# Kernel tuning notes

Hardware: AMD Instinct MI355X
Metric: run time of the kernel (lower is better)

Reference implementation:

```python
import jax, jax.numpy as jnp
import numpy as np

B, S, I, H = 64, 512, 256, 512


def setup_inputs() -> dict:
    key = jax.random.key(0)
    k1, k2, k3, k4 = jax.random.split(key, 4)
    scale = 0.1  # torch init uniform(-0.1, 0.1); we use scaled normal for randn fill
    x = jax.random.normal(k1, (B, S, I), dtype=jnp.float32)
    W = jax.random.normal(k2, (I, 4 * H), dtype=jnp.float32) * scale
    U = jax.random.normal(k3, (H, 4 * H), dtype=jnp.float32) * scale
    bias = jax.random.normal(k4, (4 * H,), dtype=jnp.float32) * scale
    return {"x": x, "W": W, "U": U, "bias": bias}


def reference(x, W, U, bias):
    bs, seq_len, _ = x.shape
    hidden = U.shape[0]
    h0 = jnp.zeros((bs, hidden), dtype=x.dtype)
    c0 = jnp.zeros((bs, hidden), dtype=x.dtype)

    # Precompute the input projection for all timesteps in one big GEMM: [B,S,4H]
    x_proj = jnp.einsum("bsi,ig->bsg", x, W) + bias

    def step(carry, xp_t):
        h_t, c_t = carry
        gates = xp_t + h_t @ U  # [B, 4H]
        i_t, f_t, g_t, o_t = jnp.split(gates, 4, axis=1)
        i_t = jax.nn.sigmoid(i_t)
        f_t = jax.nn.sigmoid(f_t)
        g_t = jnp.tanh(g_t)
        o_t = jax.nn.sigmoid(o_t)
        c_t = f_t * c_t + i_t * g_t
        h_t = o_t * jnp.tanh(c_t)
        return (h_t, c_t), h_t

    (h_f, c_f), h_seq = jax.lax.scan(step, (h0, c0), jnp.swapaxes(x_proj, 0, 1))
    hidden_seq = jnp.swapaxes(h_seq, 0, 1)  # [B, S, H]
    # dropout p=0.0 (eval) -> identity
    return hidden_seq, h_f, c_f
```

## Files before the change

### kernel.cpp

```cpp
#include <hip/hip_runtime.h>
#include <hip/hip_bf16.h>


#define BB 64
#define SS 512
#define II 256
#define HH 512
#define G4 2048
#define NGRP 4
#define GB 16
#define NWPG 16
#define NCOL 128
#define NU 32

typedef __attribute__((ext_vector_type(8))) short bf16x8;
typedef __attribute__((ext_vector_type(4))) float f32x4;
typedef unsigned long long u64t;

__device__ __forceinline__ u64t ld_llc_u64(const u64t* p) {
  return __hip_atomic_load((u64t*)p, __ATOMIC_RELAXED,
                           __HIP_MEMORY_SCOPE_AGENT);
}
__device__ __forceinline__ void st_llc_u64(u64t* p, u64t v) {
  __hip_atomic_store(p, v, __ATOMIC_RELAXED, __HIP_MEMORY_SCOPE_AGENT);
}

__global__ void convert_x_kernel(const float* __restrict__ x,
                                 __hip_bfloat16* __restrict__ xb) {
  int blk = blockIdx.x;
  int b = blk >> 9;
  int t = blk & (SS - 1);
  int i = threadIdx.x;
  xb[((size_t)t * BB + b) * II + i] = __float2bfloat16(x[(size_t)blk * II + i]);
}

__global__ void transpose_w_kernel(const float* __restrict__ W,
                                   __hip_bfloat16* __restrict__ Wt) {
  __shared__ __hip_bfloat16 tile[64][64 + 8];
  int kb = blockIdx.x & 3;
  int nb = blockIdx.x >> 2;
  int k0 = kb * 64, nb0 = nb * 64;
#pragma unroll
  for (int p = 0; p < 16; ++p) {
    int r = p * 4 + (threadIdx.x >> 6);
    int c = threadIdx.x & 63;
    tile[r][c] = __float2bfloat16(W[(size_t)(k0 + r) * G4 + nb0 + c]);
  }
  __syncthreads();
#pragma unroll
  for (int p = 0; p < 16; ++p) {
    int n = p * 4 + (threadIdx.x >> 6);
    int k = threadIdx.x & 63;
    Wt[(size_t)(nb0 + n) * II + k0 + k] = tile[k][n];
  }
}

__global__ __launch_bounds__(256, 1)
void lstm_step(const float* __restrict__ U,
               const float* __restrict__ bias,
               const __hip_bfloat16* __restrict__ xb,
               const __hip_bfloat16* __restrict__ Wt,
               u64t* __restrict__ hpub,
               unsigned* cnt,
               float* out) {
  __shared__ alignas(16) __hip_bfloat16 Ut[NCOL][HH + 8];
  __shared__ alignas(16) __hip_bfloat16 hL[GB][HH + 8];
  __shared__ float gate[GB][NCOL + 4];
  __shared__ float bia[NCOL];
  __shared__ int sh_grp, sh_w16, sh_fast;

  const int tid = threadIdx.x;

  if (tid == 0) {
    unsigned xcc;
    asm volatile("s_getreg_b32 %0, hwreg(HW_REG_XCC_ID)" : "=s"(xcc));
    xcc &= 7u;
    unsigned my = __hip_atomic_fetch_add(&cnt[xcc], 1u, __ATOMIC_RELAXED,
                                         __HIP_MEMORY_SCOPE_AGENT);
    __hip_atomic_fetch_add(&cnt[15], 1u, __ATOMIC_RELEASE,
                           __HIP_MEMORY_SCOPE_AGENT);
    while (__hip_atomic_load(&cnt[15], __ATOMIC_ACQUIRE,
                             __HIP_MEMORY_SCOPE_AGENT) < 256u) {}
    unsigned c0 = __hip_atomic_load(&cnt[0], __ATOMIC_RELAXED,
                                    __HIP_MEMORY_SCOPE_AGENT);
    unsigned c1 = __hip_atomic_load(&cnt[1], __ATOMIC_RELAXED,
                                    __HIP_MEMORY_SCOPE_AGENT);
    unsigned c2 = __hip_atomic_load(&cnt[2], __ATOMIC_RELAXED,
                                    __HIP_MEMORY_SCOPE_AGENT);
    unsigned c3 = __hip_atomic_load(&cnt[3], __ATOMIC_RELAXED,
                                    __HIP_MEMORY_SCOPE_AGENT);
    int fast = (c0 >= NWPG && c1 >= NWPG && c2 >= NWPG && c3 >= NWPG);
    int grp = -1, w16 = 0;
    if (fast) {
      if (xcc < NGRP && my < NWPG) { grp = (int)xcc; w16 = (int)my; }
    } else {
      unsigned sp = __hip_atomic_fetch_add(&cnt[9], 1u, __ATOMIC_RELAXED,
                                           __HIP_MEMORY_SCOPE_AGENT);
      if (sp < NGRP * NWPG) { grp = (int)(sp >> 4); w16 = (int)(sp & 15); }
    }
    sh_grp = grp; sh_w16 = w16; sh_fast = fast;
  }
  __syncthreads();
  const int grp = sh_grp;
  const int w16 = sh_w16;
  const bool fast = (bool)sh_fast;
  if (grp < 0) return;
  const int n0 = w16 * NU;

  for (int i = tid; i < NCOL * HH; i += 256) {
    int c = i & (NCOL - 1);
    int k = i >> 7;
    int g = c >> 5, j = c & 31;
    Ut[c][k] = __float2bfloat16(U[(size_t)k * G4 + g * HH + n0 + j]);
  }
  if (tid < NCOL) {
    int g = tid >> 5, j = tid & 31;
    bia[tid] = bias[g * HH + n0 + j];
  }
  __syncthreads();

  const int lane = tid & 63;
  const int wave = tid >> 6;
  const int l16 = lane & 15;
  const int quad = lane >> 4;
  const int c0i = (2 * wave) * 16 + l16;
  const int c1i = (2 * wave + 1) * 16 + l16;

  bf16x8 uf0[16], uf1[16];
#pragma unroll
  for (int ks = 0; ks < 16; ++ks) {
    uf0[ks] = *(const bf16x8*)(&Ut[c0i][ks * 32 + quad * 8]);
    uf1[ks] = *(const bf16x8*)(&Ut[c1i][ks * 32 + quad * 8]);
  }
  const __hip_bfloat16* wrow0 =
      Wt + (size_t)((c0i >> 5) * HH + n0 + (c0i & 31)) * II;
  const __hip_bfloat16* wrow1 =
      Wt + (size_t)((c1i >> 5) * HH + n0 + (c1i & 31)) * II;
  bf16x8 wf0[8], wf1[8];
#pragma unroll
  for (int ks = 0; ks < 8; ++ks) {
    wf0[ks] = *(const bf16x8*)(wrow0 + ks * 32 + quad * 8);
    wf1[ks] = *(const bf16x8*)(wrow1 + ks * 32 + quad * 8);
  }
  const float b0 = bia[c0i];
  const float b1 = bia[c1i];

  const int eb = (2 * tid) >> 5;
  const int ej = (2 * tid) & 31;
  float cs0 = 0.f, cs1 = 0.f;

  u64t* gbase = hpub + (size_t)grp * 2 * (GB * 256);

  bf16x8 xr[8];
  {
    const __hip_bfloat16* xrow = xb + ((size_t)0 * BB + grp * GB + l16) * II;
#pragma unroll
    for (int ks = 0; ks < 8; ++ks)
      xr[ks] = *(const bf16x8*)(xrow + ks * 32 + quad * 8);
  }
  u64t q[16];
  {
    const u64t* hr0 = gbase + (size_t)1 * (GB * 256) + tid;
#pragma unroll
    for (int k = 0; k < 16; ++k) q[k] = ld_llc_u64(hr0 + k * 256);
  }

  for (int t = 0; t < SS; ++t) {
    const u64t* hr = gbase + (size_t)((t & 1) ^ 1) * (GB * 256) + tid;
    u64t* hw = gbase + (size_t)(t & 1) * (GB * 256);
    const unsigned ewant = (unsigned)t;
    const unsigned epub = (unsigned)(t + 1);

    f32x4 acc0 = {b0, b0, b0, b0};
    f32x4 acc1 = {b1, b1, b1, b1};
#pragma unroll
    for (int ks = 0; ks < II / 32; ++ks) {
      acc0 = __builtin_amdgcn_mfma_f32_16x16x32_bf16(xr[ks], wf0[ks], acc0, 0, 0, 0);
      acc1 = __builtin_amdgcn_mfma_f32_16x16x32_bf16(xr[ks], wf1[ks], acc1, 0, 0, 0);
    }

    for (;;) {
      unsigned bad = 0;
#pragma unroll
      for (int k = 0; k < 16; ++k) bad |= ((unsigned)(q[k] >> 32) ^ ewant);
      if (bad == 0) break;
#pragma unroll
      for (int k = 0; k < 16; ++k)
        if ((unsigned)(q[k] >> 32) != ewant)
          q[k] = ld_llc_u64(hr + k * 256);
    }

#pragma unroll
    for (int k = 0; k < 16; ++k)
      *(unsigned*)(&hL[k][2 * tid]) = (unsigned)q[k];

    if (t + 1 < SS) {
      const __hip_bfloat16* xrow =
          xb + ((size_t)(t + 1) * BB + grp * GB + l16) * II;
#pragma unroll
      for (int ks = 0; ks < 8; ++ks)
        xr[ks] = *(const bf16x8*)(xrow + ks * 32 + quad * 8);
    }
    __syncthreads();

#pragma unroll
    for (int ks = 0; ks < HH / 32; ++ks) {
      bf16x8 a = *(const bf16x8*)(&hL[l16][ks * 32 + quad * 8]);
      acc0 = __builtin_amdgcn_mfma_f32_16x16x32_bf16(a, uf0[ks], acc0, 0, 0, 0);
      acc1 = __builtin_amdgcn_mfma_f32_16x16x32_bf16(a, uf1[ks], acc1, 0, 0, 0);
    }

#pragma unroll
    for (int r = 0; r < 4; ++r) {
      gate[quad * 4 + r][c0i] = acc0[r];
      gate[quad * 4 + r][c1i] = acc1[r];
    }
    __syncthreads();

    float hv[2];
#pragma unroll
    for (int s = 0; s < 2; ++s) {
      int j = ej + s;
      float& cst = s ? cs1 : cs0;
      float xi = gate[eb][j];
      float xf = gate[eb][32 + j];
      float xg = gate[eb][64 + j];
      float xo = gate[eb][96 + j];
      float it = 1.f / (1.f + __expf(-xi));
      float ft = 1.f / (1.f + __expf(-xf));
      float gx = fminf(fmaxf(xg, -15.f), 15.f);
      float eg = __expf(2.f * gx);
      float gt = (eg - 1.f) / (eg + 1.f);
      float ot = 1.f / (1.f + __expf(-xo));
      cst = ft * cst + it * gt;
      float cc = fminf(fmaxf(cst, -15.f), 15.f);
      float ec = __expf(2.f * cc);
      float th = (ec - 1.f) / (ec + 1.f);
      hv[s] = ot * th;
    }

    union { __hip_bfloat16 h2[2]; unsigned u; } hp;
    hp.h2[0] = __float2bfloat16(hv[0]);
    hp.h2[1] = __float2bfloat16(hv[1]);
    u64t pubv = ((u64t)epub << 32) | (u64t)hp.u;
    u64t* paddr = hw + eb * 256 + w16 * 16 + (ej >> 1);
    if (fast) {
      asm volatile("global_store_dwordx2 %0, %1, off sc0"
                   :: "v"(paddr), "v"(pubv) : "memory");
    } else {
      st_llc_u64(paddr, pubv);
    }
    __builtin_amdgcn_sched_barrier(0);

    if (t + 1 < SS) {
      const u64t* hrn = gbase + (size_t)(t & 1) * (GB * 256) + tid;
#pragma unroll
      for (int k = 0; k < 16; ++k) q[k] = ld_llc_u64(hrn + k * 256);
    }
    __builtin_amdgcn_sched_barrier(0);

    int bglob = grp * GB + eb;
    int hglob = n0 + ej;
    *(float2*)(out + ((size_t)bglob * SS + t) * HH + hglob) =
        make_float2(hv[0], hv[1]);
    if (t == SS - 1) {
      size_t base = (size_t)BB * SS * HH;
      *(float2*)(out + base + (size_t)bglob * HH + hglob) =
          make_float2(hv[0], hv[1]);
      *(float2*)(out + base + (size_t)BB * HH + (size_t)bglob * HH + hglob) =
          make_float2(cs0, cs1);
    }
  }
}

extern "C" void kernel_launch(void* const* d_in, const int* in_sizes, int n_in,
                              void* d_out, int out_size, void* d_ws, size_t ws_size,
                              hipStream_t stream) {
  const float* x = (const float*)d_in[0];
  const float* W = (const float*)d_in[1];
  const float* U = (const float*)d_in[2];
  const float* bias = (const float*)d_in[3];
  float* out = (float*)d_out;

  char* ws = (char*)d_ws;
  u64t* hpub = (u64t*)ws;
  __hip_bfloat16* Wt = (__hip_bfloat16*)(ws + 256 * 1024);
  __hip_bfloat16* xb =
      (__hip_bfloat16*)(ws + 256 * 1024 + (size_t)G4 * II * 2);

  unsigned* cnt = (unsigned*)((char*)d_out + out_size - 64);

  hipMemsetAsync(d_ws, 0, 256 * 1024, stream);
  hipMemsetAsync(cnt, 0, 64, stream);
  convert_x_kernel<<<BB * SS, II, 0, stream>>>(x, xb);
  transpose_w_kernel<<<128, 256, 0, stream>>>(W, Wt);
  lstm_step<<<256, 256, 0, stream>>>(U, bias, xb, Wt, hpub, cnt, out);
}
```

Baseline: 1.486 ms.

## Replace tagged h publication with per-wave flags and direct register-fed MFMA

Each h value used to carry its own epoch tag, and the group's h was staged through LDS. Now plain bf16 h is published and each wave sets a completion flag. Consumers poll 64 flags with a wave vote, then load h straight into MFMA operand registers. Gate columns are remapped so each lane gets all four gates via one lane shuffle, which removes the gate LDS buffer and both block barriers per step. The cost is a vmcnt(0) wait before each flag store, narrower 16-bit and 32-bit stores, and an extra round trip between flag poll and data load.

```diff
diff --git a/kernel.cpp b/kernel.cpp
--- a/kernel.cpp
+++ b/kernel.cpp
@@ -21,7 +21,15 @@
   return __hip_atomic_load((u64t*)p, __ATOMIC_RELAXED,
                            __HIP_MEMORY_SCOPE_AGENT);
 }
-__device__ __forceinline__ void st_llc_u64(u64t* p, u64t v) {
+__device__ __forceinline__ unsigned ld_llc_u32(const unsigned* p) {
+  return __hip_atomic_load((unsigned*)p, __ATOMIC_RELAXED,
+                           __HIP_MEMORY_SCOPE_AGENT);
+}
+__device__ __forceinline__ void st_llc_u32(unsigned* p, unsigned v) {
+  __hip_atomic_store(p, v, __ATOMIC_RELAXED, __HIP_MEMORY_SCOPE_AGENT);
+}
+__device__ __forceinline__ void st_llc_u16(unsigned short* p,
+                                           unsigned short v) {
   __hip_atomic_store(p, v, __ATOMIC_RELAXED, __HIP_MEMORY_SCOPE_AGENT);
 }
 
@@ -60,12 +68,11 @@
                const float* __restrict__ bias,
                const __hip_bfloat16* __restrict__ xb,
                const __hip_bfloat16* __restrict__ Wt,
-               u64t* __restrict__ hpub,
+               __hip_bfloat16* __restrict__ hbuf,
+               unsigned* __restrict__ flags,
                unsigned* cnt,
                float* out) {
   __shared__ alignas(16) __hip_bfloat16 Ut[NCOL][HH + 8];
-  __shared__ alignas(16) __hip_bfloat16 hL[GB][HH + 8];
-  __shared__ float gate[GB][NCOL + 4];
   __shared__ float bia[NCOL];
   __shared__ int sh_grp, sh_w16, sh_fast;
 
@@ -123,8 +130,11 @@
   const int wave = tid >> 6;
   const int l16 = lane & 15;
   const int quad = lane >> 4;
-  const int c0i = (2 * wave) * 16 + l16;
-  const int c1i = (2 * wave + 1) * 16 + l16;
+  const bool lo = (l16 < 8);
+
+  const int uloc = wave * 8 + (l16 & 7);
+  const int c0i = (lo ? 0 : 2) * 32 + uloc;
+  const int c1i = c0i + 32;
 
   bf16x8 uf0[16], uf1[16];
 #pragma unroll
@@ -145,11 +155,13 @@
   const float b0 = bia[c0i];
   const float b1 = bia[c1i];
 
-  const int eb = (2 * tid) >> 5;
-  const int ej = (2 * tid) & 31;
+  const int r0 = lo ? 0 : 2;
+  const int gu = n0 + uloc;
   float cs0 = 0.f, cs1 = 0.f;
 
-  u64t* gbase = hpub + (size_t)grp * 2 * (GB * 256);
+  __hip_bfloat16* hb0 = hbuf + (size_t)grp * 2 * GB * HH;
+  unsigned* flg = flags + grp * 64;
+  const int fid = w16 * 4 + wave;
 
   bf16x8 xr[8];
   {
@@ -158,18 +170,24 @@
     for (int ks = 0; ks < 8; ++ks)
       xr[ks] = *(const bf16x8*)(xrow + ks * 32 + quad * 8);
   }
-  u64t q[16];
-  {
-    const u64t* hr0 = gbase + (size_t)1 * (GB * 256) + tid;
-#pragma unroll
-    for (int k = 0; k < 16; ++k) q[k] = ld_llc_u64(hr0 + k * 256);
-  }
+  unsigned fpoll = 0;
 
   for (int t = 0; t < SS; ++t) {
-    const u64t* hr = gbase + (size_t)((t & 1) ^ 1) * (GB * 256) + tid;
-    u64t* hw = gbase + (size_t)(t & 1) * (GB * 256);
-    const unsigned ewant = (unsigned)t;
-    const unsigned epub = (unsigned)(t + 1);
+    const __hip_bfloat16* hbr = hb0 + (size_t)((t & 1) ^ 1) * GB * HH;
+    __hip_bfloat16* hbw = hb0 + (size_t)(t & 1) * GB * HH;
+    const unsigned want = (unsigned)t;
+
+    while (!__all((int)(fpoll >= want)))
+      fpoll = ld_llc_u32(flg + lane);
+    __builtin_amdgcn_sched_barrier(0);
+
+    const u64t* hq = (const u64t*)(hbr + (size_t)l16 * HH) + quad * 2;
+    u64t pa[16], pb[16];
+#pragma unroll
+    for (int ks = 0; ks < 16; ++ks) {
+      pa[ks] = ld_llc_u64(hq + ks * 8);
+      pb[ks] = ld_llc_u64(hq + ks * 8 + 1);
+    }
 
     f32x4 acc0 = {b0, b0, b0, b0};
     f32x4 acc1 = {b1, b1, b1, b1};
@@ -179,53 +197,27 @@
       acc1 = __builtin_amdgcn_mfma_f32_16x16x32_bf16(xr[ks], wf1[ks], acc1, 0, 0, 0);
     }
 
-    for (;;) {
-      unsigned bad = 0;
-#pragma unroll
-      for (int k = 0; k < 16; ++k) bad |= ((unsigned)(q[k] >> 32) ^ ewant);
-      if (bad == 0) break;
-#pragma unroll
-      for (int k = 0; k < 16; ++k)
-        if ((unsigned)(q[k] >> 32) != ewant)
-          q[k] = ld_llc_u64(hr + k * 256);
-    }
-
-#pragma unroll
-    for (int k = 0; k < 16; ++k)
-      *(unsigned*)(&hL[k][2 * tid]) = (unsigned)q[k];
-
-    if (t + 1 < SS) {
-      const __hip_bfloat16* xrow =
-          xb + ((size_t)(t + 1) * BB + grp * GB + l16) * II;
-#pragma unroll
-      for (int ks = 0; ks < 8; ++ks)
-        xr[ks] = *(const bf16x8*)(xrow + ks * 32 + quad * 8);
-    }
-    __syncthreads();
-
 #pragma unroll
     for (int ks = 0; ks < HH / 32; ++ks) {
-      bf16x8 a = *(const bf16x8*)(&hL[l16][ks * 32 + quad * 8]);
-      acc0 = __builtin_amdgcn_mfma_f32_16x16x32_bf16(a, uf0[ks], acc0, 0, 0, 0);
-      acc1 = __builtin_amdgcn_mfma_f32_16x16x32_bf16(a, uf1[ks], acc1, 0, 0, 0);
-    }
-
-#pragma unroll
-    for (int r = 0; r < 4; ++r) {
-      gate[quad * 4 + r][c0i] = acc0[r];
-      gate[quad * 4 + r][c1i] = acc1[r];
-    }
-    __syncthreads();
+      union { u64t a[2]; bf16x8 v; } u;
+      u.a[0] = pa[ks];
+      u.a[1] = pb[ks];
+      acc0 = __builtin_amdgcn_mfma_f32_16x16x32_bf16(u.v, uf0[ks], acc0, 0, 0, 0);
+      acc1 = __builtin_amdgcn_mfma_f32_16x16x32_bf16(u.v, uf1[ks], acc1, 0, 0, 0);
+    }
 
     float hv[2];
 #pragma unroll
     for (int s = 0; s < 2; ++s) {
-      int j = ej + s;
+      float send0 = lo ? acc0[2 + s] : acc0[s];
+      float send1 = lo ? acc1[2 + s] : acc1[s];
+      float rx0 = __shfl_xor(send0, 8, 64);
+      float rx1 = __shfl_xor(send1, 8, 64);
+      float xi = lo ? acc0[s] : rx0;
+      float xf = lo ? acc1[s] : rx1;
+      float xg = lo ? rx0 : acc0[2 + s];
+      float xo = lo ? rx1 : acc1[2 + s];
       float& cst = s ? cs1 : cs0;
-      float xi = gate[eb][j];
-      float xf = gate[eb][32 + j];
-      float xg = gate[eb][64 + j];
-      float xo = gate[eb][96 + j];
       float it = 1.f / (1.f + __expf(-xi));
       float ft = 1.f / (1.f + __expf(-xf));
       float gx = fminf(fmaxf(xg, -15.f), 15.f);
@@ -239,36 +231,42 @@
       hv[s] = ot * th;
     }
 
-    union { __hip_bfloat16 h2[2]; unsigned u; } hp;
-    hp.h2[0] = __float2bfloat16(hv[0]);
-    hp.h2[1] = __float2bfloat16(hv[1]);
-    u64t pubv = ((u64t)epub << 32) | (u64t)hp.u;
-    u64t* paddr = hw + eb * 256 + w16 * 16 + (ej >> 1);
+    union { __hip_bfloat16 h; unsigned short us; } p0, p1;
+    p0.h = __float2bfloat16(hv[0]);
+    p1.h = __float2bfloat16(hv[1]);
+    __hip_bfloat16* w0 = hbw + (size_t)(quad * 4 + r0) * HH + gu;
+    __hip_bfloat16* w1 = w0 + HH;
     if (fast) {
-      asm volatile("global_store_dwordx2 %0, %1, off sc0"
-                   :: "v"(paddr), "v"(pubv) : "memory");
+      *(unsigned short*)w0 = p0.us;
+      *(unsigned short*)w1 = p1.us;
     } else {
-      st_llc_u64(paddr, pubv);
-    }
+      st_llc_u16((unsigned short*)w0, p0.us);
+      st_llc_u16((unsigned short*)w1, p1.us);
+    }
+    asm volatile("s_waitcnt vmcnt(0)" ::: "memory");
     __builtin_amdgcn_sched_barrier(0);
+    if (lane == 0) st_llc_u32(flg + fid, (unsigned)(t + 1));
+
+    if (t + 1 < SS) fpoll = ld_llc_u32(flg + lane);
+    __builtin_amdgcn_sched_barrier(0);
 
     if (t + 1 < SS) {
-      const u64t* hrn = gbase + (size_t)(t & 1) * (GB * 256) + tid;
-#pragma unroll
-      for (int k = 0; k < 16; ++k) q[k] = ld_llc_u64(hrn + k * 256);
-    }
-    __builtin_amdgcn_sched_barrier(0);
-
-    int bglob = grp * GB + eb;
-    int hglob = n0 + ej;
-    *(float2*)(out + ((size_t)bglob * SS + t) * HH + hglob) =
-        make_float2(hv[0], hv[1]);
+      const __hip_bfloat16* xrow =
+          xb + ((size_t)(t + 1) * BB + grp * GB + l16) * II;
+#pragma unroll
+      for (int ks = 0; ks < 8; ++ks)
+        xr[ks] = *(const bf16x8*)(xrow + ks * 32 + quad * 8);
+    }
+
+    int bg0 = grp * GB + quad * 4 + r0;
+    out[((size_t)bg0 * SS + t) * HH + gu] = hv[0];
+    out[((size_t)(bg0 + 1) * SS + t) * HH + gu] = hv[1];
     if (t == SS - 1) {
       size_t base = (size_t)BB * SS * HH;
-      *(float2*)(out + base + (size_t)bglob * HH + hglob) =
-          make_float2(hv[0], hv[1]);
-      *(float2*)(out + base + (size_t)BB * HH + (size_t)bglob * HH + hglob) =
-          make_float2(cs0, cs1);
+      out[base + (size_t)bg0 * HH + gu] = hv[0];
+      out[base + (size_t)(bg0 + 1) * HH + gu] = hv[1];
+      out[base + (size_t)BB * HH + (size_t)bg0 * HH + gu] = cs0;
+      out[base + (size_t)BB * HH + (size_t)(bg0 + 1) * HH + gu] = cs1;
     }
   }
 }
@@ -283,7 +281,8 @@
   float* out = (float*)d_out;
 
   char* ws = (char*)d_ws;
-  u64t* hpub = (u64t*)ws;
+  __hip_bfloat16* hbuf = (__hip_bfloat16*)ws;
+  unsigned* flags = (unsigned*)(ws + 128 * 1024);
   __hip_bfloat16* Wt = (__hip_bfloat16*)(ws + 256 * 1024);
   __hip_bfloat16* xb =
       (__hip_bfloat16*)(ws + 256 * 1024 + (size_t)G4 * II * 2);
@@ -294,5 +293,5 @@
   hipMemsetAsync(cnt, 0, 64, stream);
   convert_x_kernel<<<BB * SS, II, 0, stream>>>(x, xb);
   transpose_w_kernel<<<128, 256, 0, stream>>>(W, Wt);
-  lstm_step<<<256, 256, 0, stream>>>(U, bias, xb, Wt, hpub, cnt, out);
-}
+  lstm_step<<<256, 256, 0, stream>>>(U, bias, xb, Wt, hbuf, flags, cnt, out);
+}
```

Measured after the change: 5.100 ms. 3.43x slower.
